# Performance work log

Hardware: AMD Instinct MI355X
Metric: run time of the kernel (lower is better)

The kernel has to match this reference:

```python
import jax, jax.numpy as jnp
import numpy as np

B, N, D, DIM = 64, 512, 128, 128
NEG_INF = -1e9


def setup_inputs() -> dict:
    key = jax.random.key(0)
    k1, k2, k3, k4 = jax.random.split(key, 4)
    atom_query = jax.random.normal(k1, (B, N, D), dtype=jnp.float32)
    # binary atom-presence mask, broadcastable over feature dim
    mask = jax.random.randint(k2, (B, N, 1), 0, 2).astype(jnp.float32)
    s = 1.0 / np.sqrt(D)
    Wq = jax.random.normal(k3, (D, DIM), dtype=jnp.float32) * s
    Wk = jax.random.normal(k4, (D, DIM), dtype=jnp.float32) * s
    bq = jnp.zeros((DIM,), dtype=jnp.float32)
    bk = jnp.zeros((DIM,), dtype=jnp.float32)
    return {"atom_query": atom_query, "mask": mask, "Wq": Wq, "bq": bq, "Wk": Wk, "bk": bk}


def reference(atom_query, mask, Wq, bq, Wk, bk):
    # projections
    q = atom_query @ Wq + bq              # [B, N, dim]
    k = atom_query @ Wk + bk              # [B, N, dim]
    mq = mask * q                          # masked query
    mk = mask * k                          # masked key

    # energy[b,i,j] = mk[b,i] . mq[b,j], with diagonal zeroed, then summed over j.
    # sum_j energy[b,i,j] = mk[b,i] . (sum_j mq[b,j]) - mk[b,i] . mq[b,i]
    # (identical math to materializing the [B,N,N] energy and reducing)
    q_sum = mq.sum(axis=1)                                   # [B, dim]
    agg = jnp.einsum('bnd,bd->bn', mk, q_sum) - (mk * mq).sum(-1)  # [B, N]
    agg = agg[:, :, None] * mask                             # [B, N, 1]

    # euclidean normalize over atom axis (tf.linalg.normalize, axis=1)
    nrm = jnp.sqrt(jnp.sum(agg * agg, axis=1, keepdims=True))
    agg = agg / nrm

    # masked softmax over atoms
    agg = agg + (1.0 - mask) * NEG_INF
    attn = jax.nn.softmax(agg, axis=1)                       # [B, N, 1]

    # v_proj=False, kq_proj=True -> values are the key projection
    context = jnp.sum(mask * attn * k, axis=1)               # [B, dim]
    return attn, context
```

## Files before the change

### kernel.cpp

```cpp
#include <hip/hip_runtime.h>
#include <math.h>

#define NB 64
#define NN 512
#define ND 128

typedef __attribute__((ext_vector_type(8))) short short8;
typedef __attribute__((ext_vector_type(4))) float f32x4;

#define KVB_OFF   0
#define QK_OFF    (NB*NN*ND/2)
#define WT_OFF    (QK_OFF + NB*NN)
#define QSUMP_OFF (WT_OFF + 16384)

__device__ inline unsigned short f2bf(float x) {
    unsigned int u = __float_as_uint(x);
    return (unsigned short)((u + 0x7FFFu + ((u >> 16) & 1u)) >> 16);
}
__device__ inline float bf2f(unsigned short u) {
    return __uint_as_float(((unsigned int)u) << 16);
}

__global__ __launch_bounds__(256) void conv_w(
    const float* __restrict__ Wq, const float* __restrict__ Wk,
    unsigned short* __restrict__ Wt)
{
    const int idx = blockIdx.x * 256 + threadIdx.x;
    const int m = idx >> 14, rem = idx & 16383;
    const int k = rem >> 7, c = rem & 127;
    const float v = m ? Wk[k*ND + c] : Wq[k*ND + c];
    Wt[(m*ND + c)*ND + k] = f2bf(v);
}

__global__ __launch_bounds__(256, 1) void proj_mfma(
    const float* __restrict__ aq, const float* __restrict__ mask,
    const unsigned short* __restrict__ Wt,
    const float* __restrict__ bq, const float* __restrict__ bk,
    unsigned short* __restrict__ kvb, float* __restrict__ qk,
    float* __restrict__ qsum_part)
{
    __shared__ __align__(16) unsigned short a_lds[128][136];
    __shared__ float mask_lds[128];
    __shared__ float qk_part[4][128];

    const int b    = blockIdx.x >> 2;
    const int m0   = (blockIdx.x & 3) << 7;
    const int t    = threadIdx.x;
    const int w    = t >> 6, lane = t & 63;
    const int quad = lane >> 4, l16 = lane & 15;

    {
        const float4* src = (const float4*)(aq + ((size_t)b*NN + m0)*ND);
        #pragma unroll
        for (int i = 0; i < 16; i++) {
            const int idx = t + 256*i;
            const int row = idx >> 5, c4 = idx & 31;
            const float4 v = src[idx];
            ushort4 o;
            o.x = f2bf(v.x); o.y = f2bf(v.y); o.z = f2bf(v.z); o.w = f2bf(v.w);
            *(ushort4*)&a_lds[row][c4*4] = o;
        }
        if (t < 128) mask_lds[t] = mask[b*NN + m0 + t];
    }

    short8 bfr[4][4];
    #pragma unroll
    for (int nt = 0; nt < 4; nt++) {
        const int col = (nt < 2) ? (w*32 + nt*16 + l16)
                                 : (ND + w*32 + (nt-2)*16 + l16);
        #pragma unroll
        for (int kc = 0; kc < 4; kc++)
            bfr[nt][kc] = *(const short8*)(Wt + col*ND + kc*32 + quad*8);
    }

    __syncthreads();

    f32x4 acc[8][4];
    #pragma unroll
    for (int m = 0; m < 8; m++)
        #pragma unroll
        for (int nt = 0; nt < 4; nt++)
            acc[m][nt] = (f32x4){0.f, 0.f, 0.f, 0.f};

    #pragma unroll
    for (int m = 0; m < 8; m++) {
        short8 afr[4];
        #pragma unroll
        for (int kc = 0; kc < 4; kc++)
            afr[kc] = *(const short8*)&a_lds[m*16 + l16][kc*32 + quad*8];
        #pragma unroll
        for (int nt = 0; nt < 4; nt++)
            #pragma unroll
            for (int kc = 0; kc < 4; kc++)
                acc[m][nt] = __builtin_amdgcn_mfma_f32_16x16x32_bf16(
                    afr[kc], bfr[nt][kc], acc[m][nt], 0, 0, 0);
    }

    float bv[4];
    #pragma unroll
    for (int nt = 0; nt < 2; nt++) bv[nt] = bq[w*32 + nt*16 + l16];
    #pragma unroll
    for (int nt = 2; nt < 4; nt++) bv[nt] = bk[w*32 + (nt-2)*16 + l16];
    #pragma unroll
    for (int m = 0; m < 8; m++)
        #pragma unroll
        for (int nt = 0; nt < 4; nt++)
            #pragma unroll
            for (int r = 0; r < 4; r++)
                acc[m][nt][r] += bv[nt];

    #pragma unroll
    for (int m = 0; m < 8; m++)
        #pragma unroll
        for (int r = 0; r < 4; r++) {
            const size_t row = (size_t)b*NN + m0 + m*16 + quad*4 + r;
            kvb[row*ND + w*32 + l16]      = f2bf(acc[m][2][r]);
            kvb[row*ND + w*32 + 16 + l16] = f2bf(acc[m][3][r]);
        }

    #pragma unroll
    for (int m = 0; m < 8; m++) {
        float p[4];
        #pragma unroll
        for (int r = 0; r < 4; r++)
            p[r] = acc[m][0][r]*acc[m][2][r] + acc[m][1][r]*acc[m][3][r];
        #pragma unroll
        for (int off = 1; off <= 8; off <<= 1)
            #pragma unroll
            for (int r = 0; r < 4; r++)
                p[r] += __shfl_xor(p[r], off);
        if (l16 == 0)
            #pragma unroll
            for (int r = 0; r < 4; r++)
                qk_part[w][m*16 + quad*4 + r] = p[r];
    }

    {
        float s0 = 0.f, s1 = 0.f;
        #pragma unroll
        for (int m = 0; m < 8; m++)
            #pragma unroll
            for (int r = 0; r < 4; r++) {
                const float mk = mask_lds[m*16 + quad*4 + r];
                s0 += mk * acc[m][0][r];
                s1 += mk * acc[m][1][r];
            }
        s0 += __shfl_xor(s0, 16); s0 += __shfl_xor(s0, 32);
        s1 += __shfl_xor(s1, 16); s1 += __shfl_xor(s1, 32);
        if (quad == 0) {
            const int slot = (b*4 + (m0 >> 7)) * ND;
            qsum_part[slot + w*32 + l16]      = s0;
            qsum_part[slot + w*32 + 16 + l16] = s1;
        }
    }

    __syncthreads();
    if (t < 128)
        qk[(size_t)b*NN + m0 + t] =
            qk_part[0][t] + qk_part[1][t] + qk_part[2][t] + qk_part[3][t];
}

__global__ __launch_bounds__(512) void fused_attn(
    const float* __restrict__ mask, const unsigned short* __restrict__ kvb,
    const float* __restrict__ qk, const float* __restrict__ qsum_part,
    float* __restrict__ out_attn, float* __restrict__ out_ctx)
{
    __shared__ float qs[128];
    __shared__ float mask_s[512];
    __shared__ float agg_s[512];
    __shared__ float red[16];
    __shared__ float bc2[2];
    __shared__ float zred[8];
    __shared__ float zbc;
    __shared__ float ctx_part[16][32];

    const int b  = blockIdx.x >> 2;
    const int cg = blockIdx.x & 3;
    const int t = threadIdx.x, w = t >> 6, lane = t & 63;
    const size_t rowbase = (size_t)b * NN;

    if (t < 128)
        qs[t] = qsum_part[(b*4 + 0)*ND + t] + qsum_part[(b*4 + 1)*ND + t]
              + qsum_part[(b*4 + 2)*ND + t] + qsum_part[(b*4 + 3)*ND + t];
    mask_s[t] = mask[rowbase + t];
    __syncthreads();

    const int h = lane & 31, half = lane >> 5;
    float qsf[4];
    #pragma unroll
    for (int j = 0; j < 4; j++) qsf[j] = qs[h*4 + j];

    for (int i0 = 0; i0 < 64; i0 += 4) {
        const int na = w*64 + i0 + half;
        const int nb2 = na + 2;
        const ushort4 ka = *(const ushort4*)(kvb + (rowbase + na)*ND + h*4);
        const ushort4 kb = *(const ushort4*)(kvb + (rowbase + nb2)*ND + h*4);
        float p0 = bf2f(ka.x)*qsf[0] + bf2f(ka.y)*qsf[1]
                 + bf2f(ka.z)*qsf[2] + bf2f(ka.w)*qsf[3];
        float p1 = bf2f(kb.x)*qsf[0] + bf2f(kb.y)*qsf[1]
                 + bf2f(kb.z)*qsf[2] + bf2f(kb.w)*qsf[3];
        #pragma unroll
        for (int off = 1; off <= 16; off <<= 1) {
            p0 += __shfl_xor(p0, off);
            p1 += __shfl_xor(p1, off);
        }
        if (h == 0) {
            agg_s[na]  = mask_s[na]  * (p0 - qk[rowbase + na]);
            agg_s[nb2] = mask_s[nb2] * (p1 - qk[rowbase + nb2]);
        }
    }
    __syncthreads();

    const float v  = agg_s[t];
    const bool um  = mask_s[t] != 0.f;
    float sq = v * v;
    float mx = um ? v : -3.0e38f;
    #pragma unroll
    for (int off = 1; off <= 32; off <<= 1) {
        sq += __shfl_xor(sq, off);
        mx = fmaxf(mx, __shfl_xor(mx, off));
    }
    if (lane == 0) { red[w] = sq; red[8 + w] = mx; }
    __syncthreads();
    if (t == 0) {
        float s = 0.f, m = -3.0e38f;
        #pragma unroll
        for (int i = 0; i < 8; i++) { s += red[i]; m = fmaxf(m, red[8 + i]); }
        bc2[0] = sqrtf(s);
        bc2[1] = m;
    }
    __syncthreads();
    const float nrm = bc2[0];
    const float M   = bc2[1];

    const float e = um ? expf((v - M) / nrm) : 0.f;
    float z = e;
    #pragma unroll
    for (int off = 1; off <= 32; off <<= 1) z += __shfl_xor(z, off);
    if (lane == 0) zred[w] = z;
    agg_s[t] = e;
    __syncthreads();
    if (t == 0) {
        float s = 0.f;
        #pragma unroll
        for (int i = 0; i < 8; i++) s += zred[i];
        zbc = s;
    }
    __syncthreads();
    const float Z = zbc;
    if (cg == 0) out_attn[rowbase + t] = e / Z;

    const int col = cg*32 + (t & 31);
    const int rg  = t >> 5;
    float a = 0.f;
    for (int n = rg; n < NN; n += 16)
        a += agg_s[n] * bf2f(kvb[(rowbase + n)*ND + col]);
    ctx_part[rg][t & 31] = a;
    __syncthreads();
    if (t < 32) {
        float s = 0.f;
        #pragma unroll
        for (int i = 0; i < 16; i++) s += ctx_part[i][t];
        out_ctx[(size_t)b*ND + cg*32 + t] = s / Z;
    }
}

extern "C" void kernel_launch(void* const* d_in, const int* in_sizes, int n_in,
                              void* d_out, int out_size, void* d_ws, size_t ws_size,
                              hipStream_t stream)
{
    const float* aq   = (const float*)d_in[0];
    const float* mask = (const float*)d_in[1];
    const float* Wq   = (const float*)d_in[2];
    const float* bq   = (const float*)d_in[3];
    const float* Wk   = (const float*)d_in[4];
    const float* bk   = (const float*)d_in[5];

    float* ws = (float*)d_ws;
    unsigned short* kvb  = (unsigned short*)(ws + KVB_OFF);
    float*          qk   = ws + QK_OFF;
    unsigned short* Wt   = (unsigned short*)(ws + WT_OFF);
    float*          qsum_part = ws + QSUMP_OFF;

    float* out_attn = (float*)d_out;
    float* out_ctx  = (float*)d_out + NB*NN;

    conv_w<<<dim3(128), dim3(256), 0, stream>>>(Wq, Wk, Wt);
    proj_mfma<<<dim3(256), dim3(256), 0, stream>>>(aq, mask, Wt, bq, bk, kvb, qk, qsum_part);
    fused_attn<<<dim3(256), dim3(512), 0, stream>>>(mask, kvb, qk, qsum_part, out_attn, out_ctx);
}
```

Before: 104.4 us.

## Fuse weight conversion, projection and attention into one cooperative kernel

Merges the three kernels into a single cooperative launch of 256 blocks of 256 threads, using a grid-wide sync between the projection phase and the attention phase. Weights are now read directly from fp32 and converted to bf16 inside each block, which removes the separate transpose kernel. The attention phase drops from 512 to 256 threads per block, so each thread handles two rows. This cuts two launch gaps but adds a grid barrier, strided uncoalesced weight loads repeated in every block, and lower parallelism in the attention phase.

```diff
diff --git a/kernel.cpp b/kernel.cpp
--- a/kernel.cpp
+++ b/kernel.cpp
@@ -1,5 +1,8 @@
 #include <hip/hip_runtime.h>
+#include <hip/hip_cooperative_groups.h>
 #include <math.h>
+
+namespace cg = cooperative_groups;
 
 #define NB 64
 #define NN 512
@@ -10,8 +13,7 @@
 
 #define KVB_OFF   0
 #define QK_OFF    (NB*NN*ND/2)
-#define WT_OFF    (QK_OFF + NB*NN)
-#define QSUMP_OFF (WT_OFF + 16384)
+#define QSUMP_OFF (QK_OFF + NB*NN)
 
 __device__ inline unsigned short f2bf(float x) {
     unsigned int u = __float_as_uint(x);
@@ -21,27 +23,27 @@
     return __uint_as_float(((unsigned int)u) << 16);
 }
 
-__global__ __launch_bounds__(256) void conv_w(
-    const float* __restrict__ Wq, const float* __restrict__ Wk,
-    unsigned short* __restrict__ Wt)
+__global__ __launch_bounds__(256, 1) void ga_all(
+    const float* __restrict__ aq, const float* __restrict__ mask,
+    const float* __restrict__ Wq, const float* __restrict__ bq,
+    const float* __restrict__ Wk, const float* __restrict__ bk,
+    unsigned short* __restrict__ kvb, float* __restrict__ qk,
+    float* __restrict__ qsum_part,
+    float* __restrict__ out_attn, float* __restrict__ out_ctx)
 {
-    const int idx = blockIdx.x * 256 + threadIdx.x;
-    const int m = idx >> 14, rem = idx & 16383;
-    const int k = rem >> 7, c = rem & 127;
-    const float v = m ? Wk[k*ND + c] : Wq[k*ND + c];
-    Wt[(m*ND + c)*ND + k] = f2bf(v);
-}
-
-__global__ __launch_bounds__(256, 1) void proj_mfma(
-    const float* __restrict__ aq, const float* __restrict__ mask,
-    const unsigned short* __restrict__ Wt,
-    const float* __restrict__ bq, const float* __restrict__ bk,
-    unsigned short* __restrict__ kvb, float* __restrict__ qk,
-    float* __restrict__ qsum_part)
-{
+    cg::grid_group grid = cg::this_grid();
+
     __shared__ __align__(16) unsigned short a_lds[128][136];
     __shared__ float mask_lds[128];
     __shared__ float qk_part[4][128];
+    __shared__ float qs[128];
+    __shared__ float mask_s[512];
+    __shared__ float agg_s[512];
+    __shared__ float red[8];
+    __shared__ float bc2[2];
+    __shared__ float zred[4];
+    __shared__ float zbc;
+    __shared__ float ctx_part[8][32];
 
     const int b    = blockIdx.x >> 2;
     const int m0   = (blockIdx.x & 3) << 7;
@@ -66,11 +68,16 @@
     short8 bfr[4][4];
     #pragma unroll
     for (int nt = 0; nt < 4; nt++) {
-        const int col = (nt < 2) ? (w*32 + nt*16 + l16)
-                                 : (ND + w*32 + (nt-2)*16 + l16);
-        #pragma unroll
-        for (int kc = 0; kc < 4; kc++)
-            bfr[nt][kc] = *(const short8*)(Wt + col*ND + kc*32 + quad*8);
+        const float* Wsrc = (nt < 2) ? Wq : Wk;
+        const int col = w*32 + (nt & 1)*16 + l16;
+        #pragma unroll
+        for (int kc = 0; kc < 4; kc++) {
+            unsigned short tmp[8];
+            #pragma unroll
+            for (int j = 0; j < 8; j++)
+                tmp[j] = f2bf(Wsrc[(kc*32 + quad*8 + j)*ND + col]);
+            bfr[nt][kc] = *(const short8*)tmp;
+        }
     }
 
     __syncthreads();
@@ -148,7 +155,7 @@
         s0 += __shfl_xor(s0, 16); s0 += __shfl_xor(s0, 32);
         s1 += __shfl_xor(s1, 16); s1 += __shfl_xor(s1, 32);
         if (quad == 0) {
-            const int slot = (b*4 + (m0 >> 7)) * ND;
+            const int slot = blockIdx.x * ND;
             qsum_part[slot + w*32 + l16]      = s0;
             qsum_part[slot + w*32 + 16 + l16] = s1;
         }
@@ -158,31 +165,18 @@
     if (t < 128)
         qk[(size_t)b*NN + m0 + t] =
             qk_part[0][t] + qk_part[1][t] + qk_part[2][t] + qk_part[3][t];
-}
-
-__global__ __launch_bounds__(512) void fused_attn(
-    const float* __restrict__ mask, const unsigned short* __restrict__ kvb,
-    const float* __restrict__ qk, const float* __restrict__ qsum_part,
-    float* __restrict__ out_attn, float* __restrict__ out_ctx)
-{
-    __shared__ float qs[128];
-    __shared__ float mask_s[512];
-    __shared__ float agg_s[512];
-    __shared__ float red[16];
-    __shared__ float bc2[2];
-    __shared__ float zred[8];
-    __shared__ float zbc;
-    __shared__ float ctx_part[16][32];
-
-    const int b  = blockIdx.x >> 2;
-    const int cg = blockIdx.x & 3;
-    const int t = threadIdx.x, w = t >> 6, lane = t & 63;
+
+    __threadfence();
+    grid.sync();
+
+    const int cg_ = blockIdx.x & 3;
     const size_t rowbase = (size_t)b * NN;
 
     if (t < 128)
         qs[t] = qsum_part[(b*4 + 0)*ND + t] + qsum_part[(b*4 + 1)*ND + t]
               + qsum_part[(b*4 + 2)*ND + t] + qsum_part[(b*4 + 3)*ND + t];
-    mask_s[t] = mask[rowbase + t];
+    mask_s[t]       = mask[rowbase + t];
+    mask_s[t + 256] = mask[rowbase + t + 256];
     __syncthreads();
 
     const int h = lane & 31, half = lane >> 5;
@@ -190,8 +184,8 @@
     #pragma unroll
     for (int j = 0; j < 4; j++) qsf[j] = qs[h*4 + j];
 
-    for (int i0 = 0; i0 < 64; i0 += 4) {
-        const int na = w*64 + i0 + half;
+    for (int i0 = 0; i0 < 128; i0 += 4) {
+        const int na  = w*128 + i0 + half;
         const int nb2 = na + 2;
         const ushort4 ka = *(const ushort4*)(kvb + (rowbase + na)*ND + h*4);
         const ushort4 kb = *(const ushort4*)(kvb + (rowbase + nb2)*ND + h*4);
@@ -211,21 +205,21 @@
     }
     __syncthreads();
 
-    const float v  = agg_s[t];
-    const bool um  = mask_s[t] != 0.f;
-    float sq = v * v;
-    float mx = um ? v : -3.0e38f;
+    const float v0 = agg_s[t], v1 = agg_s[t + 256];
+    const bool um0 = mask_s[t] != 0.f, um1 = mask_s[t + 256] != 0.f;
+    float sq = v0*v0 + v1*v1;
+    float mx = fmaxf(um0 ? v0 : -3.0e38f, um1 ? v1 : -3.0e38f);
     #pragma unroll
     for (int off = 1; off <= 32; off <<= 1) {
         sq += __shfl_xor(sq, off);
         mx = fmaxf(mx, __shfl_xor(mx, off));
     }
-    if (lane == 0) { red[w] = sq; red[8 + w] = mx; }
+    if (lane == 0) { red[w] = sq; red[4 + w] = mx; }
     __syncthreads();
     if (t == 0) {
         float s = 0.f, m = -3.0e38f;
         #pragma unroll
-        for (int i = 0; i < 8; i++) { s += red[i]; m = fmaxf(m, red[8 + i]); }
+        for (int i = 0; i < 4; i++) { s += red[i]; m = fmaxf(m, red[4 + i]); }
         bc2[0] = sqrtf(s);
         bc2[1] = m;
     }
@@ -233,35 +227,35 @@
     const float nrm = bc2[0];
     const float M   = bc2[1];
 
-    const float e = um ? expf((v - M) / nrm) : 0.f;
-    float z = e;
+    const float e0 = um0 ? expf((v0 - M) / nrm) : 0.f;
+    const float e1 = um1 ? expf((v1 - M) / nrm) : 0.f;
+    float z = e0 + e1;
     #pragma unroll
     for (int off = 1; off <= 32; off <<= 1) z += __shfl_xor(z, off);
     if (lane == 0) zred[w] = z;
-    agg_s[t] = e;
-    __syncthreads();
-    if (t == 0) {
-        float s = 0.f;
-        #pragma unroll
-        for (int i = 0; i < 8; i++) s += zred[i];
-        zbc = s;
-    }
+    agg_s[t] = e0;
+    agg_s[t + 256] = e1;
+    __syncthreads();
+    if (t == 0) zbc = zred[0] + zred[1] + zred[2] + zred[3];
     __syncthreads();
     const float Z = zbc;
-    if (cg == 0) out_attn[rowbase + t] = e / Z;
-
-    const int col = cg*32 + (t & 31);
+    if (cg_ == 0) {
+        out_attn[rowbase + t]       = e0 / Z;
+        out_attn[rowbase + t + 256] = e1 / Z;
+    }
+
+    const int col = cg_*32 + (t & 31);
     const int rg  = t >> 5;
     float a = 0.f;
-    for (int n = rg; n < NN; n += 16)
+    for (int n = rg; n < NN; n += 8)
         a += agg_s[n] * bf2f(kvb[(rowbase + n)*ND + col]);
     ctx_part[rg][t & 31] = a;
     __syncthreads();
     if (t < 32) {
         float s = 0.f;
         #pragma unroll
-        for (int i = 0; i < 16; i++) s += ctx_part[i][t];
-        out_ctx[(size_t)b*ND + cg*32 + t] = s / Z;
+        for (int i = 0; i < 8; i++) s += ctx_part[i][t];
+        out_ctx[(size_t)b*ND + cg_*32 + t] = s / Z;
     }
 }
 
@@ -277,15 +271,16 @@
     const float* bk   = (const float*)d_in[5];
 
     float* ws = (float*)d_ws;
-    unsigned short* kvb  = (unsigned short*)(ws + KVB_OFF);
-    float*          qk   = ws + QK_OFF;
-    unsigned short* Wt   = (unsigned short*)(ws + WT_OFF);
+    unsigned short* kvb       = (unsigned short*)(ws + KVB_OFF);
+    float*          qk        = ws + QK_OFF;
     float*          qsum_part = ws + QSUMP_OFF;
 
     float* out_attn = (float*)d_out;
     float* out_ctx  = (float*)d_out + NB*NN;
 
-    conv_w<<<dim3(128), dim3(256), 0, stream>>>(Wq, Wk, Wt);
-    proj_mfma<<<dim3(256), dim3(256), 0, stream>>>(aq, mask, Wt, bq, bk, kvb, qk, qsum_part);
-    fused_attn<<<dim3(256), dim3(512), 0, stream>>>(mask, kvb, qk, qsum_part, out_attn, out_ctx);
-}
+    void* args[] = { (void*)&aq, (void*)&mask, (void*)&Wq, (void*)&bq,
+                     (void*)&Wk, (void*)&bk, (void*)&kvb, (void*)&qk,
+                     (void*)&qsum_part, (void*)&out_attn, (void*)&out_ctx };
+    hipLaunchCooperativeKernel((const void*)ga_all, dim3(256), dim3(256),
+                               args, 0, stream);
+}
```

Result: slower. 190.0 us (+82.1%).

## Fuse weight bf16 conversion into projection kernel and widen attention loads

Applied to the files above, without the earlier changes.

Removes the separate conv_w launch. Each projection block now loads Wq and Wk from fp32, converts them to bf16 in shared memory and builds its MFMA B-fragments from there, reusing the LDS buffer later used for the activation tile. The attention kernel reads 8 bf16 values per lane for the q_sum dot products instead of 4, and reads 2 columns per thread in the context reduction. This saves a kernel launch and a global round trip, but every block now converts the whole weight matrix redundantly and does strided scalar LDS reads for the fragments.

```diff
diff --git a/kernel.cpp b/kernel.cpp
--- a/kernel.cpp
+++ b/kernel.cpp
@@ -10,8 +10,7 @@
 
 #define KVB_OFF   0
 #define QK_OFF    (NB*NN*ND/2)
-#define WT_OFF    (QK_OFF + NB*NN)
-#define QSUMP_OFF (WT_OFF + 16384)
+#define QSUMP_OFF (QK_OFF + NB*NN)
 
 __device__ inline unsigned short f2bf(float x) {
     unsigned int u = __float_as_uint(x);
@@ -21,25 +20,16 @@
     return __uint_as_float(((unsigned int)u) << 16);
 }
 
-__global__ __launch_bounds__(256) void conv_w(
-    const float* __restrict__ Wq, const float* __restrict__ Wk,
-    unsigned short* __restrict__ Wt)
-{
-    const int idx = blockIdx.x * 256 + threadIdx.x;
-    const int m = idx >> 14, rem = idx & 16383;
-    const int k = rem >> 7, c = rem & 127;
-    const float v = m ? Wk[k*ND + c] : Wq[k*ND + c];
-    Wt[(m*ND + c)*ND + k] = f2bf(v);
-}
-
 __global__ __launch_bounds__(256, 1) void proj_mfma(
     const float* __restrict__ aq, const float* __restrict__ mask,
-    const unsigned short* __restrict__ Wt,
-    const float* __restrict__ bq, const float* __restrict__ bk,
+    const float* __restrict__ Wq, const float* __restrict__ bq,
+    const float* __restrict__ Wk, const float* __restrict__ bk,
     unsigned short* __restrict__ kvb, float* __restrict__ qk,
     float* __restrict__ qsum_part)
 {
-    __shared__ __align__(16) unsigned short a_lds[128][136];
+    __shared__ __align__(16) unsigned char sbuf[34816];
+    unsigned short (*wst)[132] = (unsigned short (*)[132])sbuf;
+    unsigned short (*ast)[136] = (unsigned short (*)[136])sbuf;
     __shared__ float mask_lds[128];
     __shared__ float qk_part[4][128];
 
@@ -48,6 +38,40 @@
     const int t    = threadIdx.x;
     const int w    = t >> 6, lane = t & 63;
     const int quad = lane >> 4, l16 = lane & 15;
+
+    short8 bfr[4][4];
+
+    #pragma unroll
+    for (int s = 0; s < 2; s++) {
+        const float* Wsrc = s ? Wk : Wq;
+        if (s) __syncthreads();
+        {
+            const float4* src = (const float4*)Wsrc;
+            #pragma unroll
+            for (int i = 0; i < 16; i++) {
+                const int idx = t + 256*i;
+                const int row = idx >> 5, c4 = idx & 31;
+                const float4 v = src[idx];
+                ushort4 o;
+                o.x = f2bf(v.x); o.y = f2bf(v.y); o.z = f2bf(v.z); o.w = f2bf(v.w);
+                *(ushort4*)&wst[row][c4*4] = o;
+            }
+        }
+        __syncthreads();
+        #pragma unroll
+        for (int nt = 0; nt < 2; nt++) {
+            const int col = w*32 + nt*16 + l16;
+            #pragma unroll
+            for (int kc = 0; kc < 4; kc++) {
+                short8 v;
+                #pragma unroll
+                for (int j = 0; j < 8; j++)
+                    v[j] = (short)wst[kc*32 + quad*8 + j][col];
+                bfr[s*2 + nt][kc] = v;
+            }
+        }
+    }
+    __syncthreads();
 
     {
         const float4* src = (const float4*)(aq + ((size_t)b*NN + m0)*ND);
@@ -58,21 +82,10 @@
             const float4 v = src[idx];
             ushort4 o;
             o.x = f2bf(v.x); o.y = f2bf(v.y); o.z = f2bf(v.z); o.w = f2bf(v.w);
-            *(ushort4*)&a_lds[row][c4*4] = o;
+            *(ushort4*)&ast[row][c4*4] = o;
         }
         if (t < 128) mask_lds[t] = mask[b*NN + m0 + t];
     }
-
-    short8 bfr[4][4];
-    #pragma unroll
-    for (int nt = 0; nt < 4; nt++) {
-        const int col = (nt < 2) ? (w*32 + nt*16 + l16)
-                                 : (ND + w*32 + (nt-2)*16 + l16);
-        #pragma unroll
-        for (int kc = 0; kc < 4; kc++)
-            bfr[nt][kc] = *(const short8*)(Wt + col*ND + kc*32 + quad*8);
-    }
-
     __syncthreads();
 
     f32x4 acc[8][4];
@@ -87,7 +100,7 @@
         short8 afr[4];
         #pragma unroll
         for (int kc = 0; kc < 4; kc++)
-            afr[kc] = *(const short8*)&a_lds[m*16 + l16][kc*32 + quad*8];
+            afr[kc] = *(const short8*)&ast[m*16 + l16][kc*32 + quad*8];
         #pragma unroll
         for (int nt = 0; nt < 4; nt++)
             #pragma unroll
@@ -148,7 +161,7 @@
         s0 += __shfl_xor(s0, 16); s0 += __shfl_xor(s0, 32);
         s1 += __shfl_xor(s1, 16); s1 += __shfl_xor(s1, 32);
         if (quad == 0) {
-            const int slot = (b*4 + (m0 >> 7)) * ND;
+            const int slot = blockIdx.x * ND;
             qsum_part[slot + w*32 + l16]      = s0;
             qsum_part[slot + w*32 + 16 + l16] = s1;
         }
@@ -172,7 +185,7 @@
     __shared__ float bc2[2];
     __shared__ float zred[8];
     __shared__ float zbc;
-    __shared__ float ctx_part[16][32];
+    __shared__ float ctx_part[32][33];
 
     const int b  = blockIdx.x >> 2;
     const int cg = blockIdx.x & 3;
@@ -185,29 +198,22 @@
     mask_s[t] = mask[rowbase + t];
     __syncthreads();
 
-    const int h = lane & 31, half = lane >> 5;
-    float qsf[4];
-    #pragma unroll
-    for (int j = 0; j < 4; j++) qsf[j] = qs[h*4 + j];
+    const int h = lane & 15, quad = lane >> 4;
+    float qsf[8];
+    #pragma unroll
+    for (int j = 0; j < 8; j++) qsf[j] = qs[h*8 + j];
 
     for (int i0 = 0; i0 < 64; i0 += 4) {
-        const int na = w*64 + i0 + half;
-        const int nb2 = na + 2;
-        const ushort4 ka = *(const ushort4*)(kvb + (rowbase + na)*ND + h*4);
-        const ushort4 kb = *(const ushort4*)(kvb + (rowbase + nb2)*ND + h*4);
-        float p0 = bf2f(ka.x)*qsf[0] + bf2f(ka.y)*qsf[1]
-                 + bf2f(ka.z)*qsf[2] + bf2f(ka.w)*qsf[3];
-        float p1 = bf2f(kb.x)*qsf[0] + bf2f(kb.y)*qsf[1]
-                 + bf2f(kb.z)*qsf[2] + bf2f(kb.w)*qsf[3];
-        #pragma unroll
-        for (int off = 1; off <= 16; off <<= 1) {
-            p0 += __shfl_xor(p0, off);
-            p1 += __shfl_xor(p1, off);
-        }
-        if (h == 0) {
-            agg_s[na]  = mask_s[na]  * (p0 - qk[rowbase + na]);
-            agg_s[nb2] = mask_s[nb2] * (p1 - qk[rowbase + nb2]);
-        }
+        const int n = w*64 + i0 + quad;
+        const short8 kr = *(const short8*)(kvb + (rowbase + n)*ND + h*8);
+        float p = 0.f;
+        #pragma unroll
+        for (int j = 0; j < 8; j++)
+            p += bf2f((unsigned short)kr[j]) * qsf[j];
+        #pragma unroll
+        for (int off = 1; off <= 8; off <<= 1) p += __shfl_xor(p, off);
+        if (h == 0)
+            agg_s[n] = mask_s[n] * (p - qk[rowbase + n]);
     }
     __syncthreads();
 
@@ -250,17 +256,23 @@
     const float Z = zbc;
     if (cg == 0) out_attn[rowbase + t] = e / Z;
 
-    const int col = cg*32 + (t & 31);
-    const int rg  = t >> 5;
-    float a = 0.f;
-    for (int n = rg; n < NN; n += 16)
-        a += agg_s[n] * bf2f(kvb[(rowbase + n)*ND + col]);
-    ctx_part[rg][t & 31] = a;
+    const int c2  = (t & 15) * 2;
+    const int col = cg*32 + c2;
+    const int rg  = t >> 4;
+    float a0 = 0.f, a1 = 0.f;
+    for (int n = rg; n < NN; n += 32) {
+        const ushort2 kk = *(const ushort2*)(kvb + (rowbase + n)*ND + col);
+        const float ev = agg_s[n];
+        a0 += ev * bf2f(kk.x);
+        a1 += ev * bf2f(kk.y);
+    }
+    ctx_part[rg][c2]     = a0;
+    ctx_part[rg][c2 + 1] = a1;
     __syncthreads();
     if (t < 32) {
         float s = 0.f;
         #pragma unroll
-        for (int i = 0; i < 16; i++) s += ctx_part[i][t];
+        for (int i = 0; i < 32; i++) s += ctx_part[i][t];
         out_ctx[(size_t)b*ND + cg*32 + t] = s / Z;
     }
 }
@@ -277,15 +289,15 @@
     const float* bk   = (const float*)d_in[5];
 
     float* ws = (float*)d_ws;
-    unsigned short* kvb  = (unsigned short*)(ws + KVB_OFF);
-    float*          qk   = ws + QK_OFF;
-    unsigned short* Wt   = (unsigned short*)(ws + WT_OFF);
+    unsigned short* kvb       = (unsigned short*)(ws + KVB_OFF);
+    float*          qk        = ws + QK_OFF;
     float*          qsum_part = ws + QSUMP_OFF;
 
     float* out_attn = (float*)d_out;
     float* out_ctx  = (float*)d_out + NB*NN;
 
-    conv_w<<<dim3(128), dim3(256), 0, stream>>>(Wq, Wk, Wt);
-    proj_mfma<<<dim3(256), dim3(256), 0, stream>>>(aq, mask, Wt, bq, bk, kvb, qk, qsum_part);
-    fused_attn<<<dim3(256), dim3(512), 0, stream>>>(mask, kvb, qk, qsum_part, out_attn, out_ctx);
-}
+    proj_mfma<<<dim3(256), dim3(256), 0, stream>>>(aq, mask, Wq, bq, Wk, bk,
+                                                   kvb, qk, qsum_part);
+    fused_attn<<<dim3(256), dim3(512), 0, stream>>>(mask, kvb, qk, qsum_part,
+                                                    out_attn, out_ctx);
+}
```

After: 96.88 us. -7.2%, faster.
